# Optimization experiments

Measured on AMD Instinct MI355X. Metric: run time of the kernel, lower is better.

## Reference

```python
import jax, jax.numpy as jnp
from jax import lax
import numpy as np

CH = 512      # ch_in = c_in = c_out
P = 8         # p: channels per group
NG = CH // P  # depthwise groups
PG = CH // P  # pointwise groups
EPS = 1e-5
DN = ('NCHW', 'OIHW', 'NCHW')


def leaky(x):
    return jnp.where(x >= 0, x, 0.01 * x)  # LeakyReLU default slope


def setup_inputs() -> dict:
    key = jax.random.key(0)
    ks = jax.random.split(key, 8)
    N, H, W = 16, 64, 64
    return {
        'style_encoding': jax.random.normal(ks[0], (N, 512, 4, 4), jnp.float32),
        'content_in': jax.random.normal(ks[1], (N, CH, H, W), jnp.float32),
        'dw_w': jax.random.normal(ks[2], (P, 512, 2, 2), jnp.float32) * 0.05,
        'dw_b': jax.random.normal(ks[3], (P,), jnp.float32) * 0.05,
        'pk_w': jax.random.normal(ks[4], (P, 512), jnp.float32) * 0.05,
        'pk_b': jax.random.normal(ks[5], (P,), jnp.float32) * 0.05,
        'pb_w': jax.random.normal(ks[6], (CH, 512), jnp.float32) * 0.05,
        'pb_b': jax.random.normal(ks[7], (CH,), jnp.float32) * 0.05,
    }


def reference(style_encoding, content_in, dw_w, dw_b, pk_w, pk_b, pb_w, pb_b):
    N, _, H, W = content_in.shape
    # --- KernelPredictor ---
    # depthwise kernels: 2x2 valid conv on 4x4 style map -> [N, P, 3, 3]
    d = lax.conv_general_dilated(style_encoding, dw_w, (1, 1), 'VALID',
                                 dimension_numbers=DN)
    d = leaky(d + dw_b[None, :, None, None])  # [N, P, 3, 3]
    # expand: same [P,3,3] filter for every output channel -> [N, CH, P, 3, 3]
    depthwise = jnp.broadcast_to(d[:, None], (N, CH, P, 3, 3))
    # avg-pool 4 on 4x4 style map == global mean -> [N, 512]
    s_d = jnp.mean(style_encoding, axis=(2, 3))
    pk = jnp.einsum('nc,oc->no', s_d, pk_w) + pk_b       # [N, P]  (1x1 conv)
    bias = jnp.einsum('nc,oc->no', s_d, pb_w) + pb_b     # [N, CH] (1x1 conv)

    # --- per-sample grouped convs, batched by folding batch into groups ---
    padded = jnp.pad(content_in, ((0, 0), (0, 0), (1, 1), (1, 1)), mode='reflect')
    xr = padded.reshape(1, N * CH, H + 2, W + 2)
    wr = depthwise.reshape(N * CH, P, 3, 3)
    depth = lax.conv_general_dilated(xr, wr, (1, 1), 'VALID',
                                     feature_group_count=N * NG,
                                     dimension_numbers=DN)
    depth = depth.reshape(N, CH, H, W)

    # pointwise 1x1 grouped conv: weight [N, CH, P, 1, 1], identical over out
    # channels within a sample (expand); groups = PG, CH//PG == P out ch/group
    depth_g = depth.reshape(N, PG, P, H, W)
    pw_g = jnp.broadcast_to(pk[:, None, None, :], (N, PG, P, P))  # [n,g,o,j]
    out = jnp.einsum('ngjhw,ngoj->ngohw', depth_g, pw_g).reshape(N, CH, H, W)
    predicted = leaky(out + bias[:, :, None, None])

    # --- instance-norm of content (AdaIN calc_mean_std, unbiased var) ---
    mean = jnp.mean(content_in, axis=(2, 3), keepdims=True)
    std = jnp.sqrt(jnp.var(content_in, axis=(2, 3), keepdims=True, ddof=1) + EPS)
    normalized = (content_in - mean) / std
    return normalized * predicted
```

## Files before the change

kernel.cpp:

```cpp
#include <hip/hip_runtime.h>
#include <math.h>

#define PLANE 4096
#define EPS 1e-5f

typedef float f4 __attribute__((ext_vector_type(4)));

__device__ __forceinline__ float leaky(float x) { return x >= 0.f ? x : 0.01f * x; }

__device__ __forceinline__ float wave_sum(float v) {
    #pragma unroll
    for (int off = 32; off; off >>= 1) v += __shfl_xor(v, off, 64);
    return v;
}

__global__ __launch_bounds__(256) void style_kernel(
    const float* __restrict__ style,
    const float* __restrict__ dw_w,
    const float* __restrict__ dw_b,
    const float* __restrict__ pk_w,
    const float* __restrict__ pk_b,
    float* __restrict__ sd_out,
    float* __restrict__ S_out,
    float* __restrict__ d_pred)
{
    const int blk = blockIdx.x;
    const int n = blk & 15;
    const int t = threadIdx.x;
    const int wave = t >> 6, lane = t & 63;
    const float* sb = style + (size_t)n * 8192;

    if (blk < 16) {
        __shared__ float s_sd[512];
        __shared__ float red[4];
        #pragma unroll
        for (int q = 0; q < 2; ++q) {
            int c = t + 256 * q;
            const float4* sp = (const float4*)sb + c * 4;
            float4 a = sp[0], b = sp[1], d = sp[2], e = sp[3];
            float s = a.x + a.y + a.z + a.w + b.x + b.y + b.z + b.w
                    + d.x + d.y + d.z + d.w + e.x + e.y + e.z + e.w;
            s *= (1.f / 16.f);
            s_sd[c] = s;
            sd_out[n * 512 + c] = s;
        }
        __syncthreads();
        float part = 0.f;
        #pragma unroll
        for (int o = 0; o < 8; ++o)
            part += pk_w[o * 512 + t] * s_sd[t]
                  + pk_w[o * 512 + t + 256] * s_sd[t + 256];
        part = wave_sum(part);
        if (lane == 0) red[wave] = part;
        __syncthreads();
        if (t == 0) {
            float S = red[0] + red[1] + red[2] + red[3];
            #pragma unroll
            for (int o = 0; o < 8; ++o) S += pk_b[o];
            S_out[n] = S;
        }
    } else {
        const float4* wp = (const float4*)dw_w;
        for (int rr = 0; rr < 18; ++rr) {
            int r = wave * 18 + rr;
            int j = r / 9, pos = r % 9, y = pos / 3, x = pos % 3;
            float acc = 0.f;
            #pragma unroll
            for (int i = 0; i < 8; ++i) {
                int c = lane + 64 * i;
                float4 w = wp[j * 512 + c];
                const float* s = sb + c * 16 + y * 4 + x;
                acc += s[0] * w.x + s[1] * w.y + s[4] * w.z + s[5] * w.w;
            }
            acc = wave_sum(acc);
            if (lane == 0) d_pred[n * 72 + r] = leaky(acc + dw_b[j]);
        }
    }
}

__global__ __launch_bounds__(256) void fused_kernel(
    const float* __restrict__ content,
    const float* __restrict__ d_pred,
    const float* __restrict__ S_in,
    const float* __restrict__ sd,
    const float* __restrict__ pb_w,
    const float* __restrict__ pb_b,
    float* __restrict__ out)
{
    const int b = blockIdx.x;
    const int g = b & 63, n = b >> 6;
    const int t = threadIdx.x;
    const int tx = t & 15, ty = t >> 4;
    const int wave = t >> 6, lane = t & 63;

    __shared__ float s_d[72];
    __shared__ float s_S;
    __shared__ float s_bias[8], s_mean[8], s_rstd[8];
    __shared__ float reds[32], redq[32];

    if (t < 72) s_d[t] = d_pred[n * 72 + t];
    if (t == 80) s_S = S_in[n];

    {
        const int o = t >> 5, l = t & 31;
        const float* pw  = pb_w + (size_t)(g * 8 + o) * 512;
        const float* sdn = sd + n * 512;
        float acc = 0.f;
        #pragma unroll
        for (int i = 0; i < 16; ++i) acc += pw[l + 32 * i] * sdn[l + 32 * i];
        #pragma unroll
        for (int off = 16; off; off >>= 1) acc += __shfl_xor(acc, off, 64);
        if (l == 0) s_bias[o] = acc + pb_b[g * 8 + o];
    }

    const float* cbase = content + (size_t)(n * 512 + g * 8) * PLANE;

    #pragma unroll
    for (int j = 0; j < 8; ++j) {
        const float4* p = (const float4*)(cbase + j * PLANE);
        float sm = 0.f, sq = 0.f;
        #pragma unroll
        for (int k = 0; k < 4; ++k) {
            float4 v = p[k * 256 + t];
            sm += v.x + v.y + v.z + v.w;
            sq += v.x * v.x + v.y * v.y + v.z * v.z + v.w * v.w;
        }
        #pragma unroll
        for (int off = 32; off; off >>= 1) {
            sm += __shfl_xor(sm, off, 64);
            sq += __shfl_xor(sq, off, 64);
        }
        if (lane == 0) { reds[j * 4 + wave] = sm; redq[j * 4 + wave] = sq; }
    }
    __syncthreads();
    if (t < 8) {
        float S4 = reds[t * 4] + reds[t * 4 + 1] + reds[t * 4 + 2] + reds[t * 4 + 3];
        float Q4 = redq[t * 4] + redq[t * 4 + 1] + redq[t * 4 + 2] + redq[t * 4 + 3];
        float m = S4 * (1.f / 4096.f);
        float var = (Q4 - 4096.f * m * m) * (1.f / 4095.f);
        s_mean[t] = m;
        s_rstd[t] = rsqrtf(var + EPS);
    }
    __syncthreads();

    const float S = s_S;
    #pragma unroll 1
    for (int k = 0; k < 4; ++k) {
        const int h = k * 16 + ty;
        const int x0 = tx * 4;
        float D0 = 0.f, D1 = 0.f, D2 = 0.f, D3 = 0.f;
        float4 xc[8];
        #pragma unroll
        for (int j = 0; j < 8; ++j) {
            const float* cj = cbase + j * PLANE;
            #pragma unroll
            for (int r = 0; r < 3; ++r) {
                int y = h - 1 + r;
                int ry = y < 0 ? 1 : (y > 63 ? 62 : y);
                float4 v = *(const float4*)(cj + ry * 64 + x0);
                float lv = __shfl_up(v.w, 1, 64);
                float rv = __shfl_down(v.x, 1, 64);
                float xm = (tx == 0)  ? v.y : lv;
                float xp = (tx == 15) ? v.z : rv;
                const float w0 = s_d[j * 9 + r * 3 + 0];
                const float w1 = s_d[j * 9 + r * 3 + 1];
                const float w2 = s_d[j * 9 + r * 3 + 2];
                D0 += w0 * xm  + w1 * v.x + w2 * v.y;
                D1 += w0 * v.x + w1 * v.y + w2 * v.z;
                D2 += w0 * v.y + w1 * v.z + w2 * v.w;
                D3 += w0 * v.z + w1 * v.w + w2 * xp;
                if (r == 1) xc[j] = v;
            }
        }
        const float P0 = D0 * S, P1 = D1 * S, P2 = D2 * S, P3 = D3 * S;
        float* obase = out + (size_t)(n * 512 + g * 8) * PLANE + h * 64 + x0;
        #pragma unroll
        for (int o = 0; o < 8; ++o) {
            float bb = s_bias[o], m = s_mean[o], rs = s_rstd[o];
            f4 res;
            res.x = (xc[o].x - m) * rs * leaky(P0 + bb);
            res.y = (xc[o].y - m) * rs * leaky(P1 + bb);
            res.z = (xc[o].z - m) * rs * leaky(P2 + bb);
            res.w = (xc[o].w - m) * rs * leaky(P3 + bb);
            __builtin_nontemporal_store(res, (f4*)(obase + o * PLANE));
        }
    }
}

extern "C" void kernel_launch(void* const* d_in, const int* in_sizes, int n_in,
                              void* d_out, int out_size, void* d_ws, size_t ws_size,
                              hipStream_t stream) {
    const float* style   = (const float*)d_in[0];
    const float* content = (const float*)d_in[1];
    const float* dw_w    = (const float*)d_in[2];
    const float* dw_b    = (const float*)d_in[3];
    const float* pk_w    = (const float*)d_in[4];
    const float* pk_b    = (const float*)d_in[5];
    const float* pb_w    = (const float*)d_in[6];
    const float* pb_b    = (const float*)d_in[7];
    float* out = (float*)d_out;
    float* ws  = (float*)d_ws;

    const int N = 16;
    float* sd_ws  = ws;
    float* d_pred = sd_ws + N * 512;
    float* S_ws   = d_pred + N * 72;

    style_kernel<<<32, 256, 0, stream>>>(style, dw_w, dw_b, pk_w, pk_b,
                                         sd_ws, S_ws, d_pred);
    fused_kernel<<<N * 64, 256, 0, stream>>>(content, d_pred, S_ws, sd_ws,
                                             pb_w, pb_b, out);
}
```

Baseline: 309.2 us.

## Split instance-norm stats into a prep kernel and tile main kernel by row block

Per-plane mean and rstd now come from a separate prep kernel that runs one block per content plane, merged with the style-prediction work into a single launch. The main kernel no longer computes stats. Its grid grows fourfold, one block per 16-row tile of each channel group, dropping the serial four-iteration loop and adding a launch-bounds occupancy hint. The aim is far more parallel blocks and less per-block serialization, at the cost of an extra full read of content across kernels plus a small workspace round trip.

```diff
diff --git a/kernel.cpp b/kernel.cpp
--- a/kernel.cpp
+++ b/kernel.cpp
@@ -14,28 +14,57 @@
     return v;
 }
 
-__global__ __launch_bounds__(256) void style_kernel(
+__global__ __launch_bounds__(256) void prep_kernel(
     const float* __restrict__ style,
+    const float* __restrict__ content,
     const float* __restrict__ dw_w,
     const float* __restrict__ dw_b,
     const float* __restrict__ pk_w,
     const float* __restrict__ pk_b,
     float* __restrict__ sd_out,
     float* __restrict__ S_out,
-    float* __restrict__ d_pred)
+    float* __restrict__ d_pred,
+    float* __restrict__ mean_out,
+    float* __restrict__ rstd_out)
 {
     const int blk = blockIdx.x;
-    const int n = blk & 15;
     const int t = threadIdx.x;
     const int wave = t >> 6, lane = t & 63;
-    const float* sb = style + (size_t)n * 8192;
-
-    if (blk < 16) {
-        __shared__ float s_sd[512];
-        __shared__ float red[4];
-        #pragma unroll
-        for (int q = 0; q < 2; ++q) {
-            int c = t + 256 * q;
+
+    __shared__ float ls[4], lq[4];
+    __shared__ float s_sd[512];
+    __shared__ float red[4];
+
+    if (blk < 8192) {
+        const float4* base = (const float4*)(content + (size_t)blk * PLANE);
+        float s = 0.f, q = 0.f;
+        #pragma unroll
+        for (int k = 0; k < 4; ++k) {
+            float4 v = base[k * 256 + t];
+            s += v.x + v.y + v.z + v.w;
+            q += v.x * v.x + v.y * v.y + v.z * v.z + v.w * v.w;
+        }
+        #pragma unroll
+        for (int off = 32; off; off >>= 1) {
+            s += __shfl_xor(s, off, 64);
+            q += __shfl_xor(q, off, 64);
+        }
+        if (lane == 0) { ls[wave] = s; lq[wave] = q; }
+        __syncthreads();
+        if (t == 0) {
+            float S = ls[0] + ls[1] + ls[2] + ls[3];
+            float Q = lq[0] + lq[1] + lq[2] + lq[3];
+            float m = S * (1.f / 4096.f);
+            float var = (Q - 4096.f * m * m) * (1.f / 4095.f);
+            mean_out[blk] = m;
+            rstd_out[blk] = rsqrtf(var + EPS);
+        }
+    } else if (blk < 8208) {
+        const int n = blk - 8192;
+        const float* sb = style + (size_t)n * 8192;
+        #pragma unroll
+        for (int qd = 0; qd < 2; ++qd) {
+            int c = t + 256 * qd;
             const float4* sp = (const float4*)sb + c * 4;
             float4 a = sp[0], b = sp[1], d = sp[2], e = sp[3];
             float s = a.x + a.y + a.z + a.w + b.x + b.y + b.z + b.w
@@ -60,6 +89,8 @@
             S_out[n] = S;
         }
     } else {
+        const int n = blk - 8208;
+        const float* sb = style + (size_t)n * 8192;
         const float4* wp = (const float4*)dw_w;
         for (int rr = 0; rr < 18; ++rr) {
             int r = wave * 18 + rr;
@@ -78,29 +109,38 @@
     }
 }
 
-__global__ __launch_bounds__(256) void fused_kernel(
+__global__ __launch_bounds__(256, 3) void main_kernel(
     const float* __restrict__ content,
     const float* __restrict__ d_pred,
     const float* __restrict__ S_in,
     const float* __restrict__ sd,
     const float* __restrict__ pb_w,
     const float* __restrict__ pb_b,
+    const float* __restrict__ mean_in,
+    const float* __restrict__ rstd_in,
     float* __restrict__ out)
 {
-    const int b = blockIdx.x;
-    const int g = b & 63, n = b >> 6;
-    const int t = threadIdx.x;
+    const int b    = blockIdx.x;
+    const int tile = b & 3;
+    const int g    = (b >> 2) & 63;
+    const int n    = b >> 8;
+    const int t  = threadIdx.x;
     const int tx = t & 15, ty = t >> 4;
-    const int wave = t >> 6, lane = t & 63;
+    const int h  = tile * 16 + ty;
+    const int x0 = tx * 4;
 
     __shared__ float s_d[72];
     __shared__ float s_S;
     __shared__ float s_bias[8], s_mean[8], s_rstd[8];
-    __shared__ float reds[32], redq[32];
 
     if (t < 72) s_d[t] = d_pred[n * 72 + t];
     if (t == 80) s_S = S_in[n];
-
+    if (t >= 96 && t < 104) {
+        int o = t - 96;
+        int c = n * 512 + g * 8 + o;
+        s_mean[o] = mean_in[c];
+        s_rstd[o] = rstd_in[c];
+    }
     {
         const int o = t >> 5, l = t & 31;
         const float* pw  = pb_w + (size_t)(g * 8 + o) * 512;
@@ -112,78 +152,46 @@
         for (int off = 16; off; off >>= 1) acc += __shfl_xor(acc, off, 64);
         if (l == 0) s_bias[o] = acc + pb_b[g * 8 + o];
     }
+    __syncthreads();
 
     const float* cbase = content + (size_t)(n * 512 + g * 8) * PLANE;
+    float D0 = 0.f, D1 = 0.f, D2 = 0.f, D3 = 0.f;
 
     #pragma unroll
     for (int j = 0; j < 8; ++j) {
-        const float4* p = (const float4*)(cbase + j * PLANE);
-        float sm = 0.f, sq = 0.f;
-        #pragma unroll
-        for (int k = 0; k < 4; ++k) {
-            float4 v = p[k * 256 + t];
-            sm += v.x + v.y + v.z + v.w;
-            sq += v.x * v.x + v.y * v.y + v.z * v.z + v.w * v.w;
-        }
-        #pragma unroll
-        for (int off = 32; off; off >>= 1) {
-            sm += __shfl_xor(sm, off, 64);
-            sq += __shfl_xor(sq, off, 64);
-        }
-        if (lane == 0) { reds[j * 4 + wave] = sm; redq[j * 4 + wave] = sq; }
-    }
-    __syncthreads();
-    if (t < 8) {
-        float S4 = reds[t * 4] + reds[t * 4 + 1] + reds[t * 4 + 2] + reds[t * 4 + 3];
-        float Q4 = redq[t * 4] + redq[t * 4 + 1] + redq[t * 4 + 2] + redq[t * 4 + 3];
-        float m = S4 * (1.f / 4096.f);
-        float var = (Q4 - 4096.f * m * m) * (1.f / 4095.f);
-        s_mean[t] = m;
-        s_rstd[t] = rsqrtf(var + EPS);
-    }
-    __syncthreads();
+        const float* cj = cbase + j * PLANE;
+        #pragma unroll
+        for (int r = 0; r < 3; ++r) {
+            int y = h - 1 + r;
+            int ry = y < 0 ? 1 : (y > 63 ? 62 : y);
+            float4 v = *(const float4*)(cj + ry * 64 + x0);
+            float lv = __shfl_up(v.w, 1, 64);
+            float rv = __shfl_down(v.x, 1, 64);
+            float xm = (tx == 0)  ? v.y : lv;
+            float xp = (tx == 15) ? v.z : rv;
+            const float w0 = s_d[j * 9 + r * 3 + 0];
+            const float w1 = s_d[j * 9 + r * 3 + 1];
+            const float w2 = s_d[j * 9 + r * 3 + 2];
+            D0 += w0 * xm  + w1 * v.x + w2 * v.y;
+            D1 += w0 * v.x + w1 * v.y + w2 * v.z;
+            D2 += w0 * v.y + w1 * v.z + w2 * v.w;
+            D3 += w0 * v.z + w1 * v.w + w2 * xp;
+        }
+    }
 
     const float S = s_S;
-    #pragma unroll 1
-    for (int k = 0; k < 4; ++k) {
-        const int h = k * 16 + ty;
-        const int x0 = tx * 4;
-        float D0 = 0.f, D1 = 0.f, D2 = 0.f, D3 = 0.f;
-        float4 xc[8];
-        #pragma unroll
-        for (int j = 0; j < 8; ++j) {
-            const float* cj = cbase + j * PLANE;
-            #pragma unroll
-            for (int r = 0; r < 3; ++r) {
-                int y = h - 1 + r;
-                int ry = y < 0 ? 1 : (y > 63 ? 62 : y);
-                float4 v = *(const float4*)(cj + ry * 64 + x0);
-                float lv = __shfl_up(v.w, 1, 64);
-                float rv = __shfl_down(v.x, 1, 64);
-                float xm = (tx == 0)  ? v.y : lv;
-                float xp = (tx == 15) ? v.z : rv;
-                const float w0 = s_d[j * 9 + r * 3 + 0];
-                const float w1 = s_d[j * 9 + r * 3 + 1];
-                const float w2 = s_d[j * 9 + r * 3 + 2];
-                D0 += w0 * xm  + w1 * v.x + w2 * v.y;
-                D1 += w0 * v.x + w1 * v.y + w2 * v.z;
-                D2 += w0 * v.y + w1 * v.z + w2 * v.w;
-                D3 += w0 * v.z + w1 * v.w + w2 * xp;
-                if (r == 1) xc[j] = v;
-            }
-        }
-        const float P0 = D0 * S, P1 = D1 * S, P2 = D2 * S, P3 = D3 * S;
-        float* obase = out + (size_t)(n * 512 + g * 8) * PLANE + h * 64 + x0;
-        #pragma unroll
-        for (int o = 0; o < 8; ++o) {
-            float bb = s_bias[o], m = s_mean[o], rs = s_rstd[o];
-            f4 res;
-            res.x = (xc[o].x - m) * rs * leaky(P0 + bb);
-            res.y = (xc[o].y - m) * rs * leaky(P1 + bb);
-            res.z = (xc[o].z - m) * rs * leaky(P2 + bb);
-            res.w = (xc[o].w - m) * rs * leaky(P3 + bb);
-            __builtin_nontemporal_store(res, (f4*)(obase + o * PLANE));
-        }
+    const float P0 = D0 * S, P1 = D1 * S, P2 = D2 * S, P3 = D3 * S;
+    float* obase = out + (size_t)(n * 512 + g * 8) * PLANE + h * 64 + x0;
+    #pragma unroll
+    for (int o = 0; o < 8; ++o) {
+        float4 v = *(const float4*)(cbase + o * PLANE + h * 64 + x0);
+        float bb = s_bias[o], m = s_mean[o], rs = s_rstd[o];
+        f4 res;
+        res.x = (v.x - m) * rs * leaky(P0 + bb);
+        res.y = (v.y - m) * rs * leaky(P1 + bb);
+        res.z = (v.z - m) * rs * leaky(P2 + bb);
+        res.w = (v.w - m) * rs * leaky(P3 + bb);
+        __builtin_nontemporal_store(res, (f4*)(obase + o * PLANE));
     }
 }
 
@@ -202,12 +210,14 @@
     float* ws  = (float*)d_ws;
 
     const int N = 16;
-    float* sd_ws  = ws;
-    float* d_pred = sd_ws + N * 512;
-    float* S_ws   = d_pred + N * 72;
-
-    style_kernel<<<32, 256, 0, stream>>>(style, dw_w, dw_b, pk_w, pk_b,
-                                         sd_ws, S_ws, d_pred);
-    fused_kernel<<<N * 64, 256, 0, stream>>>(content, d_pred, S_ws, sd_ws,
-                                             pb_w, pb_b, out);
-}
+    float* sd_ws   = ws;
+    float* d_pred  = sd_ws + N * 512;
+    float* S_ws    = d_pred + N * 72;
+    float* mean_ws = S_ws + N;
+    float* rstd_ws = mean_ws + N * 512;
+
+    prep_kernel<<<8224, 256, 0, stream>>>(style, content, dw_w, dw_b, pk_w, pk_b,
+                                          sd_ws, S_ws, d_pred, mean_ws, rstd_ws);
+    main_kernel<<<N * 64 * 4, 256, 0, stream>>>(content, d_pred, S_ws, sd_ws,
+                                                pb_w, pb_b, mean_ws, rstd_ws, out);
+}
```

New measurement: 292.3 us. 5.4% less time.
